# Optimization experiments

Measured on AMD Instinct MI355X. Metric: run time of the kernel, lower is better.

## Reference

```python
import jax, jax.numpy as jnp
import numpy as np

B, N, M, T, D, NH = 64, 1024, 32, 8, 512, 8
OUT = 1000
NSO, NSA = N // 4, N // 8
DH = D // NH


def _conv(x, w, b):
    y = jax.lax.conv_general_dilated(x, w, (1, 1), 'SAME', dimension_numbers=('NCHW', 'OIHW', 'NCHW'))
    return y + b[None, :, None, None]


def _bn(x, g, b):
    # BatchNorm2d in train mode: per-batch statistics over (B, H, W)
    m = x.mean(axis=(0, 2, 3), keepdims=True)
    v = x.var(axis=(0, 2, 3), keepdims=True)
    return (x - m) * jax.lax.rsqrt(v + 1e-5) * g[None, :, None, None] + b[None, :, None, None]


def _mp2(x):
    b_, c, h, w = x.shape
    return x.reshape(b_, c, h // 2, 2, w // 2, 2).max(axis=(3, 5))


def _ln(x, g, b):
    m = x.mean(-1, keepdims=True)
    v = x.var(-1, keepdims=True)
    return (x - m) * jax.lax.rsqrt(v + 1e-5) * g + b


def _glu(x):
    a, b = jnp.split(x, 2, axis=-1)
    return a * jax.nn.sigmoid(b)


def setup_inputs():
    ks = iter(jax.random.split(jax.random.key(0), 64))

    def nrm(shape, fan_in):
        return jax.random.normal(next(ks), shape, jnp.float32) / np.float32(np.sqrt(fan_in))

    inp = {}
    inp['x'] = jax.random.normal(next(ks), (B, 3, 64, 64), jnp.float32)
    inp['c1w'] = nrm((16, 3, 3, 3), 27); inp['c1b'] = jnp.zeros((16,))
    inp['bn1g'] = jnp.ones((16,)); inp['bn1b'] = jnp.zeros((16,))
    inp['c2w'] = nrm((32, 16, 3, 3), 144); inp['c2b'] = jnp.zeros((32,))
    inp['bn2g'] = jnp.ones((32,)); inp['bn2b'] = jnp.zeros((32,))
    inp['c3w'] = nrm((64, 32, 3, 3), 288); inp['c3b'] = jnp.zeros((64,))
    inp['bn3g'] = jnp.ones((64,)); inp['bn3b'] = jnp.zeros((64,))
    inp['c4w'] = nrm((64, 64, 3, 3), 576); inp['c4b'] = jnp.zeros((64,))
    inp['bn4g'] = jnp.ones((64,)); inp['bn4b'] = jnp.zeros((64,))
    inp['fc1w'] = nrm((256, 256), 256); inp['fc1b'] = jnp.zeros((256,))
    inp['fc2w'] = nrm((128, D), 128); inp['fc2b'] = jnp.zeros((D,))
    inp['kvw'] = nrm((D, D), D); inp['kvb'] = jnp.zeros((D,))
    inp['kvlg'] = jnp.ones((D,)); inp['kvlb'] = jnp.zeros((D,))
    inp['synw'] = nrm((D + N, 2 * N), D + N); inp['synb'] = jnp.zeros((2 * N,))
    inp['synlg'] = jnp.ones((N,)); inp['synlb'] = jnp.zeros((N,))
    inp['nlm_w1'] = nrm((N, M, 256), M); inp['nlm_b1'] = jnp.zeros((N, 256))
    inp['nlm_w2'] = nrm((N, 128), 128); inp['nlm_b2'] = jnp.zeros((N,))
    inp['start_act'] = nrm((N,), N)
    inp['start_trace'] = nrm((N, M), N + M)
    inp['dec_a'] = jax.random.uniform(next(ks), (NSA,), jnp.float32, 0.0, 3.0)
    inp['dec_o'] = jax.random.uniform(next(ks), (NSO,), jnp.float32, 0.0, 3.0)
    inp['qw'] = nrm((NSA, D), NSA); inp['qb'] = jnp.zeros((D,))
    inp['attn_inw'] = nrm((D, 3 * D), D); inp['attn_inb'] = jnp.zeros((3 * D,))
    inp['attn_ow'] = nrm((D, D), D); inp['attn_ob'] = jnp.zeros((D,))
    inp['op_w1'] = nrm((NSO, 256), NSO); inp['op_b1'] = jnp.zeros((256,))
    inp['op_l1g'] = jnp.ones((256,)); inp['op_l1b'] = jnp.zeros((256,))
    inp['op_w2'] = nrm((256, 64), 256); inp['op_b2'] = jnp.zeros((64,))
    inp['op_l2g'] = jnp.ones((64,)); inp['op_l2b'] = jnp.zeros((64,))
    inp['op_w3'] = nrm((64, OUT), 64); inp['op_b3'] = jnp.zeros((OUT,))
    inp['aL'] = jax.random.randint(next(ks), (NSA,), 0, N)
    inp['aR'] = jax.random.randint(next(ks), (NSA,), 0, N)
    inp['oL'] = jax.random.randint(next(ks), (NSO,), 0, N)
    inp['oR'] = jax.random.randint(next(ks), (NSO,), 0, N)
    inp['task_idx'] = 0
    return inp


def _forward(x, c1w, c1b, bn1g, bn1b, c2w, c2b, bn2g, bn2b, c3w, c3b, bn3g, bn3b, c4w, c4b, bn4g, bn4b, fc1w, fc1b, fc2w, fc2b, kvw, kvb, kvlg, kvlb, synw, synb, synlg, synlb, nlm_w1, nlm_b1, nlm_w2, nlm_b2, start_act, start_trace, dec_a, dec_o, qw, qb, attn_inw, attn_inb, attn_ow, attn_ob, op_w1, op_b1, op_l1g, op_l1b, op_w2, op_b2, op_l2g, op_l2b, op_w3, op_b3, aL, aR, oL, oR):
    # --- AdaptiveCNNEncoder (3-channel branch) ---
    h = jax.nn.relu(_bn(_conv(x, c1w, c1b), bn1g, bn1b))
    h = jax.nn.relu(_bn(_conv(h, c2w, c2b), bn2g, bn2b))
    h = _mp2(h)
    h = jax.nn.relu(_bn(_conv(h, c3w, c3b), bn3g, bn3b))
    h = _mp2(h)
    h = jax.nn.relu(_bn(_conv(h, c4w, c4b), bn4g, bn4b))
    b_, c, hh, ww = h.shape
    # AdaptiveAvgPool2d((2,2)): mean over equal blocks (16x16 -> 2x2)
    h = h.reshape(b_, c, 2, hh // 2, 2, ww // 2).mean(axis=(3, 5)).reshape(b_, c * 4)
    enc = _glu(h @ fc1w + fc1b) @ fc2w + fc2b            # (B, D)
    kv = _ln(enc @ kvw + kvb, kvlg, kvlb)                # single kv token

    Wq, Wk, Wv = jnp.split(attn_inw, 3, axis=1)
    bq, bk, bv = jnp.split(attn_inb, 3)
    kh = (kv @ Wk + bk).reshape(B, NH, DH)
    vh = (kv @ Wv + bv).reshape(B, NH, DH)

    r_a = jnp.exp(-jnp.clip(dec_a, 0.0, 15.0))           # (NSA,)
    r_o = jnp.exp(-jnp.clip(dec_o, 0.0, 15.0))           # (NSO,)

    act0 = jnp.broadcast_to(start_act, (B, N))
    trace0 = jnp.broadcast_to(start_trace, (B, N, M))
    ao0 = act0[:, oL] * act0[:, oR]                      # initial out-sync accumulators
    bo0 = jnp.ones_like(ao0)
    inv_log_out = np.float32(1.0 / np.log(OUT))
    inv_sqrt_dh = np.float32(1.0 / np.sqrt(DH))

    def tick(carry, t):
        act, trace, aa, ba, ao, bo = carry
        pp = act[:, aL] * act[:, aR]
        first = (t == 0)
        aa = jnp.where(first, pp, r_a * aa + pp)
        ba = jnp.where(first, jnp.ones_like(ba), r_a * ba + 1.0)
        sync_a = aa * jax.lax.rsqrt(ba + 1e-8)
        qv = sync_a @ qw + qb
        qh = (qv @ Wq + bq).reshape(B, NH, DH)
        logits = jnp.einsum('bhd,bhd->bh', qh, kh) * inv_sqrt_dh
        w = jax.nn.softmax(logits[..., None], axis=-1)[..., 0]  # single key -> ones
        attn_out = (w[..., None] * vh).reshape(B, D) @ attn_ow + attn_ob
        pre = jnp.concatenate([attn_out, act], axis=-1)
        state = _ln(_glu(pre @ synw + synb), synlg, synlb)
        trace = jnp.concatenate([trace[:, :, 1:], state[:, :, None]], axis=-1)
        # per-neuron private MLPs, batched: (B,N,M)x(N,M,256) -> GLU -> (N,128) -> scalar
        hid = _glu(jnp.einsum('bnm,nmh->bnh', trace, nlm_w1) + nlm_b1)
        act = jnp.einsum('bnh,nh->bn', hid, nlm_w2) + nlm_b2
        po = act[:, oL] * act[:, oR]
        ao = r_o * ao + po
        bo = r_o * bo + 1.0
        sync_o = ao * jax.lax.rsqrt(bo + 1e-8)
        h1 = jax.nn.relu(_ln(sync_o @ op_w1 + op_b1, op_l1g, op_l1b))
        h2 = jax.nn.relu(_ln(h1 @ op_w2 + op_b2, op_l2g, op_l2b))
        pred = h2 @ op_w3 + op_b3
        p = jax.nn.softmax(pred, axis=-1)
        ent = -jnp.sum(p * jnp.log(p + 1e-10), axis=-1)
        ne = ent * inv_log_out
        cert = jnp.stack([ne, 1.0 - ne], axis=-1)
        return (act, trace, aa, ba, ao, bo), (pred, cert)

    carry0 = (act0, trace0, jnp.zeros((B, NSA), jnp.float32), jnp.zeros((B, NSA), jnp.float32), ao0, bo0)
    _, (preds, certs) = jax.lax.scan(tick, carry0, jnp.arange(T))
    return jnp.transpose(preds, (1, 2, 0)), jnp.transpose(certs, (1, 2, 0))


def reference(x, c1w, c1b, bn1g, bn1b, c2w, c2b, bn2g, bn2b, c3w, c3b, bn3g, bn3b, c4w, c4b, bn4g, bn4b, fc1w, fc1b, fc2w, fc2b, kvw, kvb, kvlg, kvlb, synw, synb, synlg, synlb, nlm_w1, nlm_b1, nlm_w2, nlm_b2, start_act, start_trace, dec_a, dec_o, qw, qb, attn_inw, attn_inb, attn_ow, attn_ob, op_w1, op_b1, op_l1g, op_l1b, op_w2, op_b2, op_l2g, op_l2b, op_w3, op_b3, aL, aR, oL, oR, task_idx):
    del task_idx  # single task; all task-indexed params are for task 0
    return _forward(x, c1w, c1b, bn1g, bn1b, c2w, c2b, bn2g, bn2b, c3w, c3b, bn3g, bn3b, c4w, c4b, bn4g, bn4b, fc1w, fc1b, fc2w, fc2b, kvw, kvb, kvlg, kvlb, synw, synb, synlg, synlb, nlm_w1, nlm_b1, nlm_w2, nlm_b2, start_act, start_trace, dec_a, dec_o, qw, qb, attn_inw, attn_inb, attn_ow, attn_ob, op_w1, op_b1, op_l1g, op_l1b, op_w2, op_b2, op_l2g, op_l2b, op_w3, op_b3, aL, aR, oL, oR)
```

## Files before the change

kernel.cpp:

```cpp
#include <hip/hip_runtime.h>
#include <math.h>

constexpr int B_ = 64, N_ = 1024, M_ = 32, T_ = 8;
constexpr int OUT_ = 1000, NSO_ = 256;

#define DEVFN __device__ __forceinline__

typedef __attribute__((ext_vector_type(8))) short bf16x8;
typedef __attribute__((ext_vector_type(4))) float f32x4;

DEVFN float blockReduceSum(float v, float* buf) {
  int t = threadIdx.x;
  buf[t] = v; __syncthreads();
  for (int off = blockDim.x >> 1; off > 0; off >>= 1) {
    if (t < off) buf[t] += buf[t + off];
    __syncthreads();
  }
  float r = buf[0];
  __syncthreads();
  return r;
}

DEVFN float sigmoidf_(float x) { return 1.f / (1.f + __expf(-x)); }

DEVFN unsigned short f2bf(float f) {
  unsigned u = __float_as_uint(f);
  unsigned r = (u + 0x7FFFu + ((u >> 16) & 1u)) >> 16;
  return (unsigned short)r;
}
DEVFN float bf2f(unsigned short h) { return __uint_as_float((unsigned)h << 16); }

template<int NW>
DEVFN float bsum(float v, float* red) {
  #pragma unroll
  for (int o = 32; o > 0; o >>= 1) v += __shfl_xor(v, o);
  int w = threadIdx.x >> 6, ln = threadIdx.x & 63;
  if (ln == 0) red[w] = v;
  __syncthreads();
  if (w == 0) {
    float x = (ln < NW) ? red[ln] : 0.f;
    #pragma unroll
    for (int o = 8; o > 0; o >>= 1) x += __shfl_xor(x, o);
    if (ln == 0) red[0] = x;
  }
  __syncthreads();
  float r = red[0];
  __syncthreads();
  return r;
}

template<int NW>
DEVFN float bmax(float v, float* red) {
  #pragma unroll
  for (int o = 32; o > 0; o >>= 1) v = fmaxf(v, __shfl_xor(v, o));
  int w = threadIdx.x >> 6, ln = threadIdx.x & 63;
  if (ln == 0) red[w] = v;
  __syncthreads();
  if (w == 0) {
    float x = (ln < NW) ? red[ln] : -INFINITY;
    #pragma unroll
    for (int o = 8; o > 0; o >>= 1) x = fmaxf(x, __shfl_xor(x, o));
    if (ln == 0) red[0] = x;
  }
  __syncthreads();
  float r = red[0];
  __syncthreads();
  return r;
}

__global__ __launch_bounds__(256)
void k_w1t(const float* __restrict__ w1, unsigned short* __restrict__ w1t) {
  int n = blockIdx.x;
  __shared__ float tile[32][260];
  const float* src = w1 + (size_t)n * 8192;
  for (int i = threadIdx.x; i < 8192; i += 256)
    tile[i >> 8][i & 255] = src[i];
  __syncthreads();
  int c = threadIdx.x;
  unsigned short* dst = w1t + ((size_t)n * 256 + c) * 32;
  #pragma unroll
  for (int q = 0; q < 8; ++q) {
    ushort4 o;
    o.x = f2bf(tile[q * 4 + 0][c]); o.y = f2bf(tile[q * 4 + 1][c]);
    o.z = f2bf(tile[q * 4 + 2][c]); o.w = f2bf(tile[q * 4 + 3][c]);
    *reinterpret_cast<ushort4*>(dst + q * 4) = o;
  }
}

__global__ __launch_bounds__(256)
void k_synwt(const float* __restrict__ synw2, unsigned short* __restrict__ Bt) {
  int j0 = blockIdx.x * 64, k0 = blockIdx.y * 64;
  __shared__ float tile[64][65];
  for (int i = threadIdx.x; i < 4096; i += 256) {
    int kk = i >> 6, jj = i & 63;
    tile[kk][jj] = synw2[(size_t)(k0 + kk) * 2048 + j0 + jj];
  }
  __syncthreads();
  int jj = threadIdx.x >> 2, kq = (threadIdx.x & 3) * 16;
  unsigned short* dst = Bt + (size_t)(j0 + jj) * 1024 + k0 + kq;
  #pragma unroll
  for (int q = 0; q < 4; ++q) {
    ushort4 o;
    o.x = f2bf(tile[kq + q * 4 + 0][jj]); o.y = f2bf(tile[kq + q * 4 + 1][jj]);
    o.z = f2bf(tile[kq + q * 4 + 2][jj]); o.w = f2bf(tile[kq + q * 4 + 3][jj]);
    *reinterpret_cast<ushort4*>(dst + q * 4) = o;
  }
}

template<int CIN, int COUT, int HW, int TY, int XV, int CICH, int MODE, int KSPLIT, int COSPLIT>
__global__ __launch_bounds__(256)
void k_conv_tiled(const float* __restrict__ in, const float* __restrict__ wgl,
                  const float2* __restrict__ ssin, float* __restrict__ outp) {
  constexpr int XQ = HW / XV;
  constexpr int NCG = 4;
  constexpr int CPT = COUT / (NCG * COSPLIT);
  constexpr int PADW = HW + 8;
  constexpr int NROW = TY + 2;
  constexpr int CINB = CIN / KSPLIT;
  constexpr int NCH = CINB / CICH;
  static_assert(XQ * TY == 64, "spatial threads per co-group must be 64");
  __shared__ __align__(16) float ins[CICH][NROW][PADW];

  const int b   = blockIdx.x;
  const int y0  = blockIdx.y * TY;
  const int cs  = (COSPLIT > 1) ? (int)(blockIdx.z % COSPLIT) : 0;
  const int ks  = (KSPLIT > 1) ? (int)(blockIdx.z / COSPLIT) : 0;
  const int co0 = cs * (COUT / COSPLIT);
  const int tid = threadIdx.x;
  const int sp  = tid & 63;
  const int cg  = __builtin_amdgcn_readfirstlane(tid >> 6);
  const int xq  = sp % XQ;
  const int yr  = sp / XQ;
  const int x0  = xq * XV;

  float acc[CPT][XV];
  #pragma unroll
  for (int j = 0; j < CPT; ++j)
    #pragma unroll
    for (int k = 0; k < XV; ++k) acc[j][k] = 0.f;

  for (int ch = 0; ch < NCH; ++ch) {
    const int ci0 = ks * CINB + ch * CICH;
    __syncthreads();
    constexpr int NEL = CICH * NROW * PADW;
    for (int i = tid; i < NEL; i += 256) {
      int col = i % PADW;
      int row = (i / PADW) % NROW;
      int ci  = i / (PADW * NROW);
      int gx = col - 4;
      int gy = y0 + row - 1;
      float v = 0.f;
      if (gx >= 0 && gx < HW && gy >= 0 && gy < HW) {
        if (MODE == 0) {
          v = in[((size_t)(b * CIN + ci0 + ci) * HW + gy) * HW + gx];
        } else if (MODE == 1) {
          float2 s = ssin[ci0 + ci];
          v = fmaxf(fmaf(in[((size_t)(b * CIN + ci0 + ci) * HW + gy) * HW + gx], s.x, s.y), 0.f);
        } else {
          float2 s = ssin[ci0 + ci];
          const float* p = in + ((size_t)(b * CIN + ci0 + ci) * (2 * HW) + 2 * gy) * (2 * HW) + 2 * gx;
          float v0 = fmaf(p[0],          s.x, s.y);
          float v1 = fmaf(p[1],          s.x, s.y);
          float v2 = fmaf(p[2 * HW],     s.x, s.y);
          float v3 = fmaf(p[2 * HW + 1], s.x, s.y);
          v = fmaxf(fmaxf(fmaxf(v0, v1), fmaxf(v2, v3)), 0.f);
        }
      }
      ins[ci][row][col] = v;
    }
    __syncthreads();

    for (int ci = 0; ci < CICH; ++ci) {
      const float* wci = wgl + ((size_t)(co0 + cg * CPT) * CIN + (ci0 + ci)) * 9;
      #pragma unroll
      for (int dy = 0; dy < 3; ++dy) {
        const float* r = &ins[ci][yr + dy][x0 + 4];
        float win[XV + 2];
        win[0] = r[-1];
        if constexpr (XV == 4) {
          float4 m = *reinterpret_cast<const float4*>(r);
          win[1] = m.x; win[2] = m.y; win[3] = m.z; win[4] = m.w;
        } else if constexpr (XV == 2) {
          float2 m = *reinterpret_cast<const float2*>(r);
          win[1] = m.x; win[2] = m.y;
        } else {
          win[1] = r[0];
        }
        win[XV + 1] = r[XV];
        #pragma unroll
        for (int j = 0; j < CPT; ++j) {
          const float* wj = wci + (size_t)j * CIN * 9 + dy * 3;
          float w0 = wj[0], w1 = wj[1], w2 = wj[2];
          #pragma unroll
          for (int k = 0; k < XV; ++k)
            acc[j][k] = fmaf(win[k], w0, fmaf(win[k + 1], w1, fmaf(win[k + 2], w2, acc[j][k])));
        }
      }
    }
  }

  const size_t pofs = (size_t)ks * B_ * COUT * HW * HW;
  #pragma unroll
  for (int j = 0; j < CPT; ++j) {
    float* op = outp + pofs + (((size_t)b * COUT + co0 + cg * CPT + j) * HW + y0 + yr) * HW + x0;
    if constexpr (XV == 4)
      *reinterpret_cast<float4*>(op) = make_float4(acc[j][0], acc[j][1], acc[j][2], acc[j][3]);
    else if constexpr (XV == 2)
      *reinterpret_cast<float2*>(op) = make_float2(acc[j][0], acc[j][1]);
    else
      *op = acc[j][0];
  }
}

template<int C, int HW2, int NS>
__global__ __launch_bounds__(256)
void k_bn_stats(const float* __restrict__ x, float* __restrict__ part) {
  int c = blockIdx.x, s = blockIdx.y, ns = gridDim.y;
  const int Npc = B_ * HW2;
  constexpr size_t PSTR = (size_t)B_ * C * HW2;
  float s1 = 0.f, s2 = 0.f;
  for (int ii = s * 256 + threadIdx.x; ii < Npc; ii += ns * 256) {
    int b = ii / HW2, pos = ii % HW2;
    size_t base = ((size_t)b * C + c) * HW2 + pos;
    float v = x[base];
    #pragma unroll
    for (int q = 1; q < NS; ++q) v += x[base + q * PSTR];
    s1 += v; s2 += v * v;
  }
  __shared__ float r1[256], r2[256];
  r1[threadIdx.x] = s1; r2[threadIdx.x] = s2; __syncthreads();
  for (int off = 128; off > 0; off >>= 1) {
    if (threadIdx.x < off) { r1[threadIdx.x] += r1[threadIdx.x + off]; r2[threadIdx.x] += r2[threadIdx.x + off]; }
    __syncthreads();
  }
  if (threadIdx.x == 0) {
    part[(c * ns + s) * 2 + 0] = r1[0];
    part[(c * ns + s) * 2 + 1] = r2[0];
  }
}

__global__ void k_bn_finalize(const float* __restrict__ part, int C, int ns, float inv_n,
                              const float* __restrict__ g, const float* __restrict__ bb,
                              float2* __restrict__ ss) {
  int c = threadIdx.x;
  if (c >= C) return;
  float s1 = 0.f, s2 = 0.f;
  for (int s = 0; s < ns; ++s) { s1 += part[(c * ns + s) * 2]; s2 += part[(c * ns + s) * 2 + 1]; }
  float m = s1 * inv_n;
  float var = s2 * inv_n - m * m;
  float rstd = rsqrtf(var + 1e-5f);
  float sc = g[c] * rstd;
  ss[c] = make_float2(sc, bb[c] - m * sc);
}

__global__ __launch_bounds__(256)
void k_avgpool_bn(const float* __restrict__ x, const float2* __restrict__ ss,
                  float* __restrict__ outp) {
  constexpr size_t PSTR = (size_t)B_ * 64 * 256;
  int idx = blockIdx.x * 256 + threadIdx.x;
  if (idx >= B_ * 256) return;
  int b = idx >> 8;
  int r = idx & 255;
  int c = r >> 2, i = (r >> 1) & 1, j = r & 1;
  float2 s = ss[c];
  const float* p = x + ((size_t)(b * 64 + c) * 16 + i * 8) * 16 + j * 8;
  float sum = 0.f;
  #pragma unroll
  for (int yy = 0; yy < 8; ++yy)
    #pragma unroll
    for (int xx = 0; xx < 8; ++xx) {
      size_t o = yy * 16 + xx;
      float v = p[o] + p[o + PSTR] + p[o + 2 * PSTR] + p[o + 3 * PSTR];
      sum += fmaxf(fmaf(v, s.x, s.y), 0.f);
    }
  outp[idx] = sum * (1.f / 64.f);
}

template<int K, int NOUT>
__global__ __launch_bounds__(256)
void k_gemm_part(const float* __restrict__ A, const float* __restrict__ W, int ldw,
                 float* __restrict__ part) {
  int jt = blockIdx.x, ks = blockIdx.y;
  int k0 = ks * 64;
  __shared__ float As[64][65];
  for (int i = threadIdx.x; i < 4096; i += 256) {
    int r = i >> 6, c = i & 63;
    As[r][c] = A[(size_t)r * K + k0 + c];
  }
  __syncthreads();
  int jsub = threadIdx.x & 31;
  int bg = threadIdx.x >> 5;
  int j = jt * 32 + jsub;
  float acc[8] = {0.f, 0.f, 0.f, 0.f, 0.f, 0.f, 0.f, 0.f};
  const float* wp = W + (size_t)k0 * ldw + j;
  #pragma unroll 8
  for (int kk = 0; kk < 64; ++kk) {
    float w = wp[(size_t)kk * ldw];
    #pragma unroll
    for (int r = 0; r < 8; ++r) acc[r] = fmaf(As[bg * 8 + r][kk], w, acc[r]);
  }
  float* pp = part + (size_t)ks * 64 * NOUT + j;
  #pragma unroll
  for (int r = 0; r < 8; ++r) pp[(size_t)(bg * 8 + r) * NOUT] = acc[r];
}

__global__ __launch_bounds__(256)
void k_syn_mfma(const unsigned short* __restrict__ Abf, const unsigned short* __restrict__ Bt,
                float* __restrict__ part) {
  const int jt = blockIdx.x, ks = blockIdx.y;
  const int w = threadIdx.x >> 6, lane = threadIdx.x & 63;
  const int col = lane & 15, kg = lane >> 4;
  const int jcol = jt * 64 + w * 16 + col;
  const int k0 = ks * 256;
  f32x4 acc[4];
  #pragma unroll
  for (int mt = 0; mt < 4; ++mt) acc[mt] = (f32x4){0.f, 0.f, 0.f, 0.f};

  #pragma unroll
  for (int kb = 0; kb < 8; ++kb) {
    const int kk = k0 + kb * 32 + kg * 8;
    bf16x8 bfr = *reinterpret_cast<const bf16x8*>(Bt + (size_t)jcol * 1024 + kk);
    #pragma unroll
    for (int mt = 0; mt < 4; ++mt) {
      bf16x8 a = *reinterpret_cast<const bf16x8*>(Abf + (size_t)(mt * 16 + col) * 1024 + kk);
      acc[mt] = __builtin_amdgcn_mfma_f32_16x16x32_bf16(a, bfr, acc[mt], 0, 0, 0);
    }
  }
  #pragma unroll
  for (int mt = 0; mt < 4; ++mt) {
    int b0 = mt * 16 + kg * 4;
    #pragma unroll
    for (int r = 0; r < 4; ++r)
      part[((size_t)ks * 64 + b0 + r) * 2048 + jcol] = acc[mt][r];
  }
}

template<int NOUT, int NO_FIN, int KS, bool GLU_, bool LN_>
__global__ __launch_bounds__(256)
void k_fc_reduce(const float* __restrict__ part, const float* __restrict__ bias, int bstride,
                 const float* __restrict__ lng, const float* __restrict__ lnb,
                 float* __restrict__ outp) {
  constexpr int R = (NO_FIN + 255) / 256;
  int b = blockIdx.x, t = threadIdx.x;
  const float* bp = bias + (size_t)b * bstride;
  float v[R];
  #pragma unroll
  for (int r = 0; r < R; ++r) {
    int j = t + r * 256;
    if (j < NO_FIN) {
      float za = bp[j];
      float zb = GLU_ ? bp[j + NO_FIN] : 0.f;
      #pragma unroll
      for (int ks = 0; ks < KS; ++ks) {
        const float* pr = part + ((size_t)ks * 64 + b) * NOUT;
        za += pr[j];
        if (GLU_) zb += pr[j + NO_FIN];
      }
      v[r] = GLU_ ? za * sigmoidf_(zb) : za;
    } else v[r] = 0.f;
  }
  if (LN_) {
    __shared__ float red[256];
    float s1 = 0.f, s2 = 0.f;
    #pragma unroll
    for (int r = 0; r < R; ++r) { s1 += v[r]; s2 += v[r] * v[r]; }
    s1 = blockReduceSum(s1, red);
    s2 = blockReduceSum(s2, red);
    float mu = s1 / (float)NO_FIN;
    float rstd = rsqrtf(s2 / (float)NO_FIN - mu * mu + 1e-5f);
    #pragma unroll
    for (int r = 0; r < R; ++r) {
      int j = t + r * 256;
      if (j < NO_FIN) outp[(size_t)b * NO_FIN + j] = fmaf((v[r] - mu) * rstd, lng[j], lnb[j]);
    }
  } else {
    #pragma unroll
    for (int r = 0; r < R; ++r) {
      int j = t + r * 256;
      if (j < NO_FIN) outp[(size_t)b * NO_FIN + j] = v[r];
    }
  }
}

__global__ __launch_bounds__(1024)
void k_syn_reduce(const float* __restrict__ part, const float* __restrict__ syncst,
                  const float* __restrict__ g, const float* __restrict__ bb,
                  unsigned short* __restrict__ trace, int slot) {
  int b = blockIdx.x, t = threadIdx.x;
  __shared__ float red[16];
  float za = syncst[b * 2048 + t];
  float zb = syncst[b * 2048 + 1024 + t];
  #pragma unroll
  for (int ks = 0; ks < 4; ++ks) {
    const float* pr = part + ((size_t)ks * 64 + b) * 2048;
    za += pr[t];
    zb += pr[t + 1024];
  }
  float v = za * sigmoidf_(zb);
  float s1 = bsum<16>(v, red);
  float s2 = bsum<16>(v * v, red);
  float mu = s1 * (1.f / 1024.f);
  float rstd = rsqrtf(s2 * (1.f / 1024.f) - mu * mu + 1e-5f);
  trace[((size_t)t * 64 + b) * 32 + slot] = f2bf(fmaf((v - mu) * rstd, g[t], bb[t]));
}

__global__ __launch_bounds__(256)
void k_init(const float* __restrict__ sa, const float* __restrict__ st,
            const int* __restrict__ oL, const int* __restrict__ oR,
            float* __restrict__ act, unsigned short* __restrict__ act_bf,
            unsigned short* __restrict__ trace,
            float* __restrict__ ao, float* __restrict__ bo) {
  int idx = blockIdx.x * 256 + threadIdx.x;
  if (idx < B_ * N_ * M_) {
    int n = idx >> 11, m = idx & 31;
    trace[idx] = f2bf(st[n * 32 + m]);
  }
  if (idx < B_ * N_) {
    float v = sa[idx % N_];
    act[idx] = v;
    act_bf[idx] = f2bf(v);
  }
  if (idx < B_ * NSO_) {
    int i = idx % NSO_;
    ao[idx] = sa[oL[i]] * sa[oR[i]];
    bo[idx] = 1.f;
  }
}

__global__ __launch_bounds__(128)
void k_nlm_mfma(const unsigned short* __restrict__ trace, const unsigned short* __restrict__ w1t,
                const float* __restrict__ b1, const float* __restrict__ w2,
                const float* __restrict__ b2, float* __restrict__ act,
                unsigned short* __restrict__ act_bf, int tick) {
  const int w = threadIdx.x >> 6, lane = threadIdx.x & 63;
  const int n = blockIdx.x * 2 + w;
  const int col = lane & 15, kg = lane >> 4;
  __shared__ __align__(16) unsigned short ldsA[2][64][40];
  {
    const uint4* src = reinterpret_cast<const uint4*>(trace + ((size_t)n * 64 + lane) * 32);
    uint4 r0 = src[0], r1 = src[1], r2 = src[2], r3 = src[3];
    uint4* d = reinterpret_cast<uint4*>(&ldsA[w][lane][0]);
    d[0] = r0; d[1] = r1; d[2] = r2; d[3] = r3;
  }
  bf16x8 bf[16];
  float b1v[16], w2v[8];
  #pragma unroll
  for (int nt = 0; nt < 16; ++nt) {
    bf[nt] = *reinterpret_cast<const bf16x8*>(w1t + (((size_t)n * 256 + nt * 16 + col) * 32 + kg * 8));
    b1v[nt] = b1[n * 256 + nt * 16 + col];
  }
  #pragma unroll
  for (int nt = 0; nt < 8; ++nt) w2v[nt] = w2[n * 128 + nt * 16 + col];
  const float b2n = b2[n];
  const int kbase = kg * 8 + ((tick + 1) & 31);
  __syncthreads();
  #pragma unroll
  for (int mt = 0; mt < 4; ++mt) {
    const int brow = mt * 16 + col;
    bf16x8 af;
    #pragma unroll
    for (int j = 0; j < 8; ++j)
      af[j] = (short)ldsA[w][brow][(kbase + j) & 31];
    f32x4 acc[16];
    #pragma unroll
    for (int nt = 0; nt < 16; ++nt)
      acc[nt] = __builtin_amdgcn_mfma_f32_16x16x32_bf16(af, bf[nt], (f32x4){0.f, 0.f, 0.f, 0.f}, 0, 0, 0);
    float v0 = 0.f, v1 = 0.f, v2 = 0.f, v3 = 0.f;
    #pragma unroll
    for (int nt = 0; nt < 8; ++nt) {
      f32x4 za = acc[nt], zb = acc[nt + 8];
// ... 18 lines not shown
      act_bf[(size_t)(b0 + 0) * 1024 + n] = f2bf(r0);
      act_bf[(size_t)(b0 + 1) * 1024 + n] = f2bf(r1);
      act_bf[(size_t)(b0 + 2) * 1024 + n] = f2bf(r2);
      act_bf[(size_t)(b0 + 3) * 1024 + n] = f2bf(r3);
    }
  }
}

__global__ __launch_bounds__(1024)
void k_outpath(const float* __restrict__ act, float* __restrict__ ao, float* __restrict__ bo,
               const float* __restrict__ dec_o, const int* __restrict__ oL, const int* __restrict__ oR,
               const float* __restrict__ opw1, const float* __restrict__ opb1,
               const float* __restrict__ l1g, const float* __restrict__ l1b,
               const float* __restrict__ opw2, const float* __restrict__ opb2,
               const float* __restrict__ l2g, const float* __restrict__ l2b,
               const float* __restrict__ opw3, const float* __restrict__ opb3,
               float* __restrict__ outp, int tick) {
  int b = blockIdx.x, t = threadIdx.x;
  __shared__ float red[16];
  __shared__ float syo[256], h1s[256], h2s[64];
  __shared__ float zp1[4][256];
  __shared__ float zp2[16][64];
  const float* actb = act + (size_t)b * 1024;
  if (t < 256) {
    float po = actb[oL[t]] * actb[oR[t]];
    float r = __expf(-fminf(fmaxf(dec_o[t], 0.f), 15.f));
    int ai = b * 256 + t;
    float av = fmaf(r, ao[ai], po);
    float bv = fmaf(r, bo[ai], 1.f);
    ao[ai] = av; bo[ai] = bv;
    syo[t] = av * rsqrtf(bv + 1e-8f);
  }
  __syncthreads();
  {
    int j = t & 255, ks = t >> 8;
    float z = 0.f;
    const float* wcol = opw1 + j;
    #pragma unroll 8
    for (int k = ks * 64; k < ks * 64 + 64; ++k) z = fmaf(syo[k], wcol[k * 256], z);
    zp1[ks][j] = z;
  }
  __syncthreads();
  float h1v = 0.f;
  if (t < 256) h1v = zp1[0][t] + zp1[1][t] + zp1[2][t] + zp1[3][t] + opb1[t];
  float s1 = bsum<16>(t < 256 ? h1v : 0.f, red);
  float s2 = bsum<16>(t < 256 ? h1v * h1v : 0.f, red);
  if (t < 256) {
    float mu = s1 * (1.f / 256.f);
    float rstd = rsqrtf(s2 * (1.f / 256.f) - mu * mu + 1e-5f);
    h1s[t] = fmaxf(fmaf((h1v - mu) * rstd, l1g[t], l1b[t]), 0.f);
  }
  __syncthreads();
  {
    int j = t & 63, ks = t >> 6;
    float z = 0.f;
    const float* wcol = opw2 + j;
    #pragma unroll
    for (int k = ks * 16; k < ks * 16 + 16; ++k) z = fmaf(h1s[k], wcol[k * 64], z);
    zp2[ks][j] = z;
  }
  __syncthreads();
  if (t < 64) {
    float z2 = opb2[t];
    #pragma unroll
    for (int ks = 0; ks < 16; ++ks) z2 += zp2[ks][t];
    float a1 = z2, a2 = z2 * z2;
    #pragma unroll
    for (int o = 32; o > 0; o >>= 1) { a1 += __shfl_xor(a1, o); a2 += __shfl_xor(a2, o); }
    float mu2 = a1 * (1.f / 64.f);
    float rs2 = rsqrtf(a2 * (1.f / 64.f) - mu2 * mu2 + 1e-5f);
    h2s[t] = fmaxf(fmaf((z2 - mu2) * rs2, l2g[t], l2b[t]), 0.f);
  }
  __syncthreads();
  float z3 = 0.f;
  if (t < OUT_) {
    z3 = opb3[t];
    const float* wcol = opw3 + t;
    #pragma unroll 8
    for (int k = 0; k < 64; ++k) z3 = fmaf(h2s[k], wcol[k * OUT_], z3);
    outp[(size_t)b * (OUT_ * T_) + (size_t)t * T_ + tick] = z3;
  }
  float mx = bmax<16>(t < OUT_ ? z3 : -INFINITY, red);
  float e = (t < OUT_) ? __expf(z3 - mx) : 0.f;
  float S = bsum<16>(e, red);
  float inv = 1.f / S;
  float ep = 0.f;
  if (t < OUT_) {
    float p = e * inv;
    ep = p * __logf(p + 1e-10f);
  }
  float ent = -bsum<16>(ep, red);
  if (t == 0) {
    float ne = ent * (1.f / logf(1000.f));
    outp[(size_t)B_ * OUT_ * T_ + (size_t)b * 2 * T_ + tick]      = ne;
    outp[(size_t)B_ * OUT_ * T_ + (size_t)b * 2 * T_ + T_ + tick] = 1.f - ne;
  }
}

extern "C" void kernel_launch(void* const* d_in, const int* in_sizes, int n_in,
                              void* d_out, int out_size, void* d_ws, size_t ws_size,
                              hipStream_t stream) {
  (void)in_sizes; (void)n_in; (void)out_size; (void)ws_size;
  const float* x      = (const float*)d_in[0];
  const float* c1w    = (const float*)d_in[1];
  const float* bn1g   = (const float*)d_in[3];
  const float* bn1b   = (const float*)d_in[4];
  const float* c2w    = (const float*)d_in[5];
  const float* bn2g   = (const float*)d_in[7];
  const float* bn2b   = (const float*)d_in[8];
  const float* c3w    = (const float*)d_in[9];
  const float* bn3g   = (const float*)d_in[11];
  const float* bn3b   = (const float*)d_in[12];
  const float* c4w    = (const float*)d_in[13];
  const float* bn4g   = (const float*)d_in[15];
  const float* bn4b   = (const float*)d_in[16];
  const float* fc1w   = (const float*)d_in[17];
  const float* fc1b   = (const float*)d_in[18];
  const float* fc2w   = (const float*)d_in[19];
  const float* fc2b   = (const float*)d_in[20];
  const float* kvw    = (const float*)d_in[21];
  const float* kvb    = (const float*)d_in[22];
  const float* kvlg   = (const float*)d_in[23];
  const float* kvlb   = (const float*)d_in[24];
  const float* synw   = (const float*)d_in[25];
  const float* synb   = (const float*)d_in[26];
  const float* synlg  = (const float*)d_in[27];
  const float* synlb  = (const float*)d_in[28];
  const float* nlmw1  = (const float*)d_in[29];
  const float* nlmb1  = (const float*)d_in[30];
  const float* nlmw2  = (const float*)d_in[31];
  const float* nlmb2  = (const float*)d_in[32];
  const float* sact   = (const float*)d_in[33];
  const float* strc   = (const float*)d_in[34];
  const float* dec_o  = (const float*)d_in[36];
  const float* attn_inw = (const float*)d_in[39];
  const float* attn_inb = (const float*)d_in[40];
  const float* attn_ow  = (const float*)d_in[41];
  const float* attn_ob  = (const float*)d_in[42];
  const float* opw1   = (const float*)d_in[43];
  const float* opb1   = (const float*)d_in[44];
  const float* opl1g  = (const float*)d_in[45];
  const float* opl1b  = (const float*)d_in[46];
  const float* opw2   = (const float*)d_in[47];
  const float* opb2   = (const float*)d_in[48];
  const float* opl2g  = (const float*)d_in[49];
  const float* opl2b  = (const float*)d_in[50];
  const float* opw3   = (const float*)d_in[51];
  const float* opb3   = (const float*)d_in[52];
  const int*   oL     = (const int*)d_in[55];
  const int*   oR     = (const int*)d_in[56];
  float* outp = (float*)d_out;
  float* ws   = (float*)d_ws;

  float* c2raw = ws;
  float* c4part= ws;
  float* c1raw = ws + 8388608;
  float* c3raw = ws + 8388608;
  float* part  = ws + 4194304;
  unsigned short* trace_bf = (unsigned short*)(ws + 6291456);
  float* act   = ws + 8388608;
  float* syncst= ws + 8454144;
  float* pooled= ws + 8585216;
  float* ench  = ws + 8601600;
  float* enc   = ws + 8609792;
  float* kvbuf = ws + 8642560;
  float* vhbuf = ws + 8675328;
  float* aout  = ws + 8708096;
  float* ao    = ws + 8740864;
  float* bo    = ws + 8757248;
  unsigned short* w1t_bf   = (unsigned short*)(ws + 8777728);
  unsigned short* synw2t_bf= (unsigned short*)(ws + 12972032);
  float* bnpart= ws + 14020608;
  float2* bnss = (float2*)(ws + 14024704);
  unsigned short* act_bf = (unsigned short*)(ws + 14028800);

  k_conv_tiled<3,16,64,4,4,3,0,1,1><<<dim3(64,16),256,0,stream>>>(x, c1w, nullptr, c1raw);
  k_bn_stats<16,4096,1><<<dim3(16,32),256,0,stream>>>(c1raw, bnpart);
  k_bn_finalize<<<1,64,0,stream>>>(bnpart, 16, 32, 1.f/(float)(B_*4096), bn1g, bn1b, bnss);

  k_conv_tiled<16,32,64,2,2,16,1,1,1><<<dim3(64,32),256,0,stream>>>(c1raw, c2w, bnss, c2raw);
  k_bn_stats<32,4096,1><<<dim3(32,32),256,0,stream>>>(c2raw, bnpart);
  k_bn_finalize<<<1,64,0,stream>>>(bnpart, 32, 32, 1.f/(float)(B_*4096), bn2g, bn2b, bnss);

  k_conv_tiled<32,64,32,4,2,16,2,1,2><<<dim3(64,8,2),256,0,stream>>>(c2raw, c3w, bnss, c3raw);
  k_bn_stats<64,1024,1><<<dim3(64,16),256,0,stream>>>(c3raw, bnpart);
  k_bn_finalize<<<1,64,0,stream>>>(bnpart, 64, 16, 1.f/(float)(B_*1024), bn3g, bn3b, bnss);

  k_conv_tiled<64,64,16,4,1,16,2,4,1><<<dim3(64,4,4),256,0,stream>>>(c3raw, c4w, bnss, c4part);

  k_w1t<<<1024,256,0,stream>>>(nlmw1, w1t_bf);
  k_synwt<<<dim3(32,16),256,0,stream>>>(synw + (size_t)512 * 2048, synw2t_bf);

  k_bn_stats<64,256,4><<<dim3(64,8),256,0,stream>>>(c4part, bnpart);
  k_bn_finalize<<<1,64,0,stream>>>(bnpart, 64, 8, 1.f/(float)(B_*256), bn4g, bn4b, bnss);
  k_avgpool_bn<<<64,256,0,stream>>>(c4part, bnss, pooled);

  k_gemm_part<256,256><<<dim3(8,4),256,0,stream>>>(pooled, fc1w, 256, part);
  k_fc_reduce<256,128,4,true,false><<<64,256,0,stream>>>(part, fc1b, 0, nullptr, nullptr, ench);
  k_gemm_part<128,512><<<dim3(16,2),256,0,stream>>>(ench, fc2w, 512, part);
  k_fc_reduce<512,512,2,false,false><<<64,256,0,stream>>>(part, fc2b, 0, nullptr, nullptr, enc);
  k_gemm_part<512,512><<<dim3(16,8),256,0,stream>>>(enc, kvw, 512, part);
  k_fc_reduce<512,512,8,false,true><<<64,256,0,stream>>>(part, kvb, 0, kvlg, kvlb, kvbuf);
  k_gemm_part<512,512><<<dim3(16,8),256,0,stream>>>(kvbuf, attn_inw + 1024, 1536, part);
  k_fc_reduce<512,512,8,false,false><<<64,256,0,stream>>>(part, attn_inb + 1024, 0, nullptr, nullptr, vhbuf);
  k_gemm_part<512,512><<<dim3(16,8),256,0,stream>>>(vhbuf, attn_ow, 512, part);
  k_fc_reduce<512,512,8,false,false><<<64,256,0,stream>>>(part, attn_ob, 0, nullptr, nullptr, aout);
  k_gemm_part<512,2048><<<dim3(64,8),256,0,stream>>>(aout, synw, 2048, part);
  k_fc_reduce<2048,2048,8,false,false><<<64,256,0,stream>>>(part, synb, 0, nullptr, nullptr, syncst);

  k_init<<<8192,256,0,stream>>>(sact, strc, oL, oR, act, act_bf, trace_bf, ao, bo);

  for (int t = 0; t < T_; ++t) {
    k_syn_mfma<<<dim3(32,4),256,0,stream>>>(act_bf, synw2t_bf, part);
    k_syn_reduce<<<64,1024,0,stream>>>(part, syncst, synlg, synlb, trace_bf, t);
    k_nlm_mfma<<<512,128,0,stream>>>(trace_bf, w1t_bf, nlmb1, nlmw2, nlmb2, act, act_bf, t);
    k_outpath<<<64,1024,0,stream>>>(act, ao, bo, dec_o, oL, oR,
                                    opw1, opb1, opl1g, opl1b,
                                    opw2, opb2, opl2g, opl2b,
                                    opw3, opb3, outp, t);
  }
}
```

Baseline: 595.2 us.

## Move conv2-4 to bf16 MFMA implicit GEMM with bf16 activations

```diff
diff --git a/kernel.cpp b/kernel.cpp
--- a/kernel.cpp
+++ b/kernel.cpp
@@ -68,6 +68,38 @@
   return r;
 }
 
+DEVFN void bn_ssl(float2* ssl, const float* bnpart, const float* g, const float* bb,
+                  int C, int ns, float inv_n) {
+  for (int c = threadIdx.x; c < C; c += blockDim.x) {
+    float s1 = 0.f, s2 = 0.f;
+    for (int s = 0; s < ns; ++s) { s1 += bnpart[(c * ns + s) * 2]; s2 += bnpart[(c * ns + s) * 2 + 1]; }
+    float m = s1 * inv_n;
+    float var = s2 * inv_n - m * m;
+    float rstd = rsqrtf(var + 1e-5f);
+    float sc = g[c] * rstd;
+    ssl[c] = make_float2(sc, bb[c] - m * sc);
+  }
+}
+
+__global__ __launch_bounds__(256)
+void k_wprep(const float* __restrict__ c2w, const float* __restrict__ c3w,
+             const float* __restrict__ c4w, unsigned short* __restrict__ wt2,
+             unsigned short* __restrict__ wt3, unsigned short* __restrict__ wt4) {
+  int i = blockIdx.x * 256 + threadIdx.x;
+  if (i < 5120) {
+    int tap = i / 512, co = (i / 16) % 32, ci = i & 15;
+    wt2[i] = (tap < 9) ? f2bf(c2w[(co * 16 + ci) * 9 + tap]) : 0;
+  } else if (i < 5120 + 18432) {
+    int j = i - 5120;
+    int tap = j / 2048, co = (j / 32) % 64, ci = j & 31;
+    wt3[j] = f2bf(c3w[(co * 32 + ci) * 9 + tap]);
+  } else if (i < 5120 + 18432 + 36864) {
+    int j = i - 5120 - 18432;
+    int tap = j / 4096, co = (j / 64) % 64, ci = j & 63;
+    wt4[j] = f2bf(c4w[(co * 64 + ci) * 9 + tap]);
+  }
+}
+
 __global__ __launch_bounds__(256)
 void k_w1t(const float* __restrict__ w1, unsigned short* __restrict__ w1t) {
   int n = blockIdx.x;
@@ -107,125 +139,221 @@
   }
 }
 
-template<int CIN, int COUT, int HW, int TY, int XV, int CICH, int MODE, int KSPLIT, int COSPLIT>
-__global__ __launch_bounds__(256)
-void k_conv_tiled(const float* __restrict__ in, const float* __restrict__ wgl,
-                  const float2* __restrict__ ssin, float* __restrict__ outp) {
-  constexpr int XQ = HW / XV;
-  constexpr int NCG = 4;
-  constexpr int CPT = COUT / (NCG * COSPLIT);
-  constexpr int PADW = HW + 8;
-  constexpr int NROW = TY + 2;
-  constexpr int CINB = CIN / KSPLIT;
-  constexpr int NCH = CINB / CICH;
-  static_assert(XQ * TY == 64, "spatial threads per co-group must be 64");
-  __shared__ __align__(16) float ins[CICH][NROW][PADW];
-
-  const int b   = blockIdx.x;
-  const int y0  = blockIdx.y * TY;
-  const int cs  = (COSPLIT > 1) ? (int)(blockIdx.z % COSPLIT) : 0;
-  const int ks  = (KSPLIT > 1) ? (int)(blockIdx.z / COSPLIT) : 0;
-  const int co0 = cs * (COUT / COSPLIT);
+__global__ __launch_bounds__(256)
+void k_conv1(const float* __restrict__ in, const float* __restrict__ wgl,
+             unsigned short* __restrict__ outp) {
+  constexpr int HW = 64, TY = 4, XV = 4, XQ = 16, CPT = 4;
+  __shared__ __align__(16) float ins[3][TY + 2][HW + 8];
+  const int b = blockIdx.x, y0 = blockIdx.y * TY, tid = threadIdx.x;
+  const int sp = tid & 63;
+  const int cg = __builtin_amdgcn_readfirstlane(tid >> 6);
+  const int xq = sp % XQ, yr = sp / XQ, x0 = xq * XV;
+  float acc[CPT][XV];
+  #pragma unroll
+  for (int j = 0; j < CPT; ++j)
+    #pragma unroll
+    for (int k = 0; k < XV; ++k) acc[j][k] = 0.f;
+  constexpr int NEL = 3 * (TY + 2) * (HW + 8);
+  for (int i = tid; i < NEL; i += 256) {
+    int col = i % (HW + 8), row = (i / (HW + 8)) % (TY + 2), ci = i / ((HW + 8) * (TY + 2));
+    int gx = col - 4, gy = y0 + row - 1;
+    float v = 0.f;
+    if (gx >= 0 && gx < HW && gy >= 0 && gy < HW)
+      v = in[((size_t)(b * 3 + ci) * HW + gy) * HW + gx];
+    ins[ci][row][col] = v;
+  }
+  __syncthreads();
+  for (int ci = 0; ci < 3; ++ci) {
+    const float* wci = wgl + ((size_t)(cg * CPT) * 3 + ci) * 9;
+    #pragma unroll
+    for (int dy = 0; dy < 3; ++dy) {
+      const float* r = &ins[ci][yr + dy][x0 + 4];
+      float win[6];
+      win[0] = r[-1];
+      float4 m = *reinterpret_cast<const float4*>(r);
+      win[1] = m.x; win[2] = m.y; win[3] = m.z; win[4] = m.w;
+      win[5] = r[4];
+      #pragma unroll
+      for (int j = 0; j < CPT; ++j) {
+        const float* wj = wci + (size_t)j * 27 + dy * 3;
+        float w0 = wj[0], w1 = wj[1], w2 = wj[2];
+        #pragma unroll
+        for (int k = 0; k < XV; ++k)
+          acc[j][k] = fmaf(win[k], w0, fmaf(win[k + 1], w1, fmaf(win[k + 2], w2, acc[j][k])));
+      }
+    }
+  }
+  #pragma unroll
+  for (int j = 0; j < CPT; ++j) {
+    unsigned short* op = outp + (((size_t)b * 16 + cg * CPT + j) * HW + y0 + yr) * HW + x0;
+    ushort4 o;
+    o.x = f2bf(acc[j][0]); o.y = f2bf(acc[j][1]); o.z = f2bf(acc[j][2]); o.w = f2bf(acc[j][3]);
+    *reinterpret_cast<ushort4*>(op) = o;
+  }
+}
+
+__global__ __launch_bounds__(256)
+void k_conv2_mfma(const unsigned short* __restrict__ in, const unsigned short* __restrict__ wt2,
+                  const float* __restrict__ bnpart, const float* __restrict__ bng,
+                  const float* __restrict__ bnb, unsigned short* __restrict__ outp) {
+  const int b = blockIdx.x, y = blockIdx.y;
   const int tid = threadIdx.x;
-  const int sp  = tid & 63;
-  const int cg  = __builtin_amdgcn_readfirstlane(tid >> 6);
-  const int xq  = sp % XQ;
-  const int yr  = sp / XQ;
-  const int x0  = xq * XV;
-
-  float acc[CPT][XV];
-  #pragma unroll
-  for (int j = 0; j < CPT; ++j)
-    #pragma unroll
-    for (int k = 0; k < XV; ++k) acc[j][k] = 0.f;
-
-  for (int ch = 0; ch < NCH; ++ch) {
-    const int ci0 = ks * CINB + ch * CICH;
-    __syncthreads();
-    constexpr int NEL = CICH * NROW * PADW;
-    for (int i = tid; i < NEL; i += 256) {
-      int col = i % PADW;
-      int row = (i / PADW) % NROW;
-      int ci  = i / (PADW * NROW);
-      int gx = col - 4;
-      int gy = y0 + row - 1;
-      float v = 0.f;
-      if (gx >= 0 && gx < HW && gy >= 0 && gy < HW) {
-        if (MODE == 0) {
-          v = in[((size_t)(b * CIN + ci0 + ci) * HW + gy) * HW + gx];
-        } else if (MODE == 1) {
-          float2 s = ssin[ci0 + ci];
-          v = fmaxf(fmaf(in[((size_t)(b * CIN + ci0 + ci) * HW + gy) * HW + gx], s.x, s.y), 0.f);
-        } else {
-          float2 s = ssin[ci0 + ci];
-          const float* p = in + ((size_t)(b * CIN + ci0 + ci) * (2 * HW) + 2 * gy) * (2 * HW) + 2 * gx;
-          float v0 = fmaf(p[0],          s.x, s.y);
-          float v1 = fmaf(p[1],          s.x, s.y);
-          float v2 = fmaf(p[2 * HW],     s.x, s.y);
-          float v3 = fmaf(p[2 * HW + 1], s.x, s.y);
-          v = fmaxf(fmaxf(fmaxf(v0, v1), fmaxf(v2, v3)), 0.f);
-        }
+  const int w = tid >> 6, lane = tid & 63;
+  const int col = lane & 15, kg = lane >> 4;
+  const int p0 = w * 16;
+  __shared__ unsigned short lds[3][68][16];
+  __shared__ float2 ssl[16];
+  bn_ssl(ssl, bnpart, bng, bnb, 16, 32, 1.f / (float)(B_ * 4096));
+  __syncthreads();
+  for (int i = tid; i < 3 * 66 * 16; i += 256) {
+    int px = i % 66, row = (i / 66) % 3, ci = i / 198;
+    int gy = y + row - 1, gx = px - 1;
+    float v = 0.f;
+    if (gy >= 0 && gy < 64 && gx >= 0 && gx < 64) {
+      float2 s = ssl[ci];
+      v = fmaxf(fmaf(bf2f(in[((size_t)(b * 16 + ci) * 64 + gy) * 64 + gx]), s.x, s.y), 0.f);
+    }
+    lds[row][px][ci] = f2bf(v);
+  }
+  __syncthreads();
+  f32x4 acc0 = {0.f, 0.f, 0.f, 0.f}, acc1 = {0.f, 0.f, 0.f, 0.f};
+  const int tsel = kg >> 1, ci0 = (kg & 1) * 8;
+  #pragma unroll
+  for (int p = 0; p < 5; ++p) {
+    int tap = 2 * p + tsel;
+    int dy = (tap < 9) ? tap / 3 : 0;
+    int dx = (tap < 9) ? tap % 3 : 0;
+    bf16x8 af = *reinterpret_cast<const bf16x8*>(&lds[dy][p0 + col + dx][ci0]);
+    bf16x8 b0 = *reinterpret_cast<const bf16x8*>(wt2 + ((size_t)tap * 32 + col) * 16 + ci0);
+    bf16x8 b1 = *reinterpret_cast<const bf16x8*>(wt2 + ((size_t)tap * 32 + 16 + col) * 16 + ci0);
+    acc0 = __builtin_amdgcn_mfma_f32_16x16x32_bf16(af, b0, acc0, 0, 0, 0);
+    acc1 = __builtin_amdgcn_mfma_f32_16x16x32_bf16(af, b1, acc1, 0, 0, 0);
+  }
+  int px = p0 + kg * 4;
+  ushort4 o0, o1;
+  o0.x = f2bf(acc0[0]); o0.y = f2bf(acc0[1]); o0.z = f2bf(acc0[2]); o0.w = f2bf(acc0[3]);
+  o1.x = f2bf(acc1[0]); o1.y = f2bf(acc1[1]); o1.z = f2bf(acc1[2]); o1.w = f2bf(acc1[3]);
+  *reinterpret_cast<ushort4*>(outp + ((size_t)(b * 32 + col) * 64 + y) * 64 + px) = o0;
+  *reinterpret_cast<ushort4*>(outp + ((size_t)(b * 32 + 16 + col) * 64 + y) * 64 + px) = o1;
+}
+
+__global__ __launch_bounds__(256)
+void k_conv3_mfma(const unsigned short* __restrict__ in, const unsigned short* __restrict__ wt3,
+                  const float* __restrict__ bnpart, const float* __restrict__ bng,
+                  const float* __restrict__ bnb, unsigned short* __restrict__ outp) {
+  const int b = blockIdx.x, y0 = blockIdx.y * 2;
+  const int tid = threadIdx.x;
+  const int w = tid >> 6, lane = tid & 63;
+  const int col = lane & 15, kg = lane >> 4;
+  const int yloc = w >> 1, p0 = (w & 1) * 16;
+  __shared__ unsigned short lds[4][34][40];
+  __shared__ float2 ssl[32];
+  bn_ssl(ssl, bnpart, bng, bnb, 32, 32, 1.f / (float)(B_ * 4096));
+  __syncthreads();
+  for (int i = tid; i < 4 * 34 * 32; i += 256) {
+    int px = i % 34, row = (i / 34) % 4, ci = i / 136;
+    int gy = y0 + row - 1, gx = px - 1;
+    float v = 0.f;
+    if (gy >= 0 && gy < 32 && gx >= 0 && gx < 32) {
+      float2 s = ssl[ci];
+      size_t base = ((size_t)(b * 32 + ci) * 64 + 2 * gy) * 64 + 2 * gx;
+      float r0 = fmaf(bf2f(in[base]),      s.x, s.y);
+      float r1 = fmaf(bf2f(in[base + 1]),  s.x, s.y);
+      float r2 = fmaf(bf2f(in[base + 64]), s.x, s.y);
+      float r3 = fmaf(bf2f(in[base + 65]), s.x, s.y);
+      v = fmaxf(fmaxf(fmaxf(r0, r1), fmaxf(r2, r3)), 0.f);
+    }
+    lds[row][px][ci] = f2bf(v);
+  }
+  __syncthreads();
+  f32x4 acc[4];
+  #pragma unroll
+  for (int c = 0; c < 4; ++c) acc[c] = (f32x4){0.f, 0.f, 0.f, 0.f};
+  #pragma unroll
+  for (int tap = 0; tap < 9; ++tap) {
+    int dy = tap / 3, dx = tap % 3;
+    bf16x8 af = *reinterpret_cast<const bf16x8*>(&lds[yloc + dy][p0 + col + dx][kg * 8]);
+    #pragma unroll
+    for (int c = 0; c < 4; ++c) {
+      bf16x8 bfr = *reinterpret_cast<const bf16x8*>(wt3 + ((size_t)tap * 64 + c * 16 + col) * 32 + kg * 8);
+      acc[c] = __builtin_amdgcn_mfma_f32_16x16x32_bf16(af, bfr, acc[c], 0, 0, 0);
+    }
+  }
+  int yy = y0 + yloc, px = p0 + kg * 4;
+  #pragma unroll
+  for (int c = 0; c < 4; ++c) {
+    ushort4 o;
+    o.x = f2bf(acc[c][0]); o.y = f2bf(acc[c][1]); o.z = f2bf(acc[c][2]); o.w = f2bf(acc[c][3]);
+    *reinterpret_cast<ushort4*>(outp + ((size_t)(b * 64 + c * 16 + col) * 32 + yy) * 32 + px) = o;
+  }
+}
+
+__global__ __launch_bounds__(128)
+void k_conv4_mfma(const unsigned short* __restrict__ in, const unsigned short* __restrict__ wt4,
+                  const float* __restrict__ bnpart, const float* __restrict__ bng,
+                  const float* __restrict__ bnb, unsigned short* __restrict__ outp) {
+  const int b = blockIdx.x, y0 = blockIdx.y * 2;
+  const int tid = threadIdx.x;
+  const int w = tid >> 6, lane = tid & 63;
+  const int col = lane & 15, kg = lane >> 4;
+  __shared__ unsigned short lds[4][18][72];
+  __shared__ float2 ssl[64];
+  bn_ssl(ssl, bnpart, bng, bnb, 64, 16, 1.f / (float)(B_ * 1024));
+  __syncthreads();
+  for (int i = tid; i < 4 * 18 * 64; i += 128) {
+    int px = i % 18, row = (i / 18) % 4, ci = i / 72;
+    int gy = y0 + row - 1, gx = px - 1;
+    float v = 0.f;
+    if (gy >= 0 && gy < 16 && gx >= 0 && gx < 16) {
+      float2 s = ssl[ci];
+      size_t base = ((size_t)(b * 64 + ci) * 32 + 2 * gy) * 32 + 2 * gx;
+      float r0 = fmaf(bf2f(in[base]),      s.x, s.y);
+      float r1 = fmaf(bf2f(in[base + 1]),  s.x, s.y);
+      float r2 = fmaf(bf2f(in[base + 32]), s.x, s.y);
+      float r3 = fmaf(bf2f(in[base + 33]), s.x, s.y);
+      v = fmaxf(fmaxf(fmaxf(r0, r1), fmaxf(r2, r3)), 0.f);
+    }
+    lds[row][px][ci] = f2bf(v);
+  }
+  __syncthreads();
+  f32x4 acc[4];
+  #pragma unroll
+  for (int c = 0; c < 4; ++c) acc[c] = (f32x4){0.f, 0.f, 0.f, 0.f};
+  #pragma unroll
+  for (int tap = 0; tap < 9; ++tap) {
+    int dy = tap / 3, dx = tap % 3;
+    #pragma unroll
+    for (int kc = 0; kc < 2; ++kc) {
+      bf16x8 af = *reinterpret_cast<const bf16x8*>(&lds[w + dy][col + dx][kc * 32 + kg * 8]);
+      #pragma unroll
+      for (int c = 0; c < 4; ++c) {
+        bf16x8 bfr = *reinterpret_cast<const bf16x8*>(wt4 + ((size_t)tap * 64 + c * 16 + col) * 64 + kc * 32 + kg * 8);
+        acc[c] = __builtin_amdgcn_mfma_f32_16x16x32_bf16(af, bfr, acc[c], 0, 0, 0);
       }
-      ins[ci][row][col] = v;
-    }
-    __syncthreads();
-
-    for (int ci = 0; ci < CICH; ++ci) {
-      const float* wci = wgl + ((size_t)(co0 + cg * CPT) * CIN + (ci0 + ci)) * 9;
-      #pragma unroll
-      for (int dy = 0; dy < 3; ++dy) {
-        const float* r = &ins[ci][yr + dy][x0 + 4];
-        float win[XV + 2];
-        win[0] = r[-1];
-        if constexpr (XV == 4) {
-          float4 m = *reinterpret_cast<const float4*>(r);
-          win[1] = m.x; win[2] = m.y; win[3] = m.z; win[4] = m.w;
-        } else if constexpr (XV == 2) {
-          float2 m = *reinterpret_cast<const float2*>(r);
-          win[1] = m.x; win[2] = m.y;
-        } else {
-          win[1] = r[0];
-        }
-        win[XV + 1] = r[XV];
-        #pragma unroll
-        for (int j = 0; j < CPT; ++j) {
-          const float* wj = wci + (size_t)j * CIN * 9 + dy * 3;
-          float w0 = wj[0], w1 = wj[1], w2 = wj[2];
-          #pragma unroll
-          for (int k = 0; k < XV; ++k)
-            acc[j][k] = fmaf(win[k], w0, fmaf(win[k + 1], w1, fmaf(win[k + 2], w2, acc[j][k])));
-        }
-      }
-    }
-  }
-
-  const size_t pofs = (size_t)ks * B_ * COUT * HW * HW;
-  #pragma unroll
-  for (int j = 0; j < CPT; ++j) {
-    float* op = outp + pofs + (((size_t)b * COUT + co0 + cg * CPT + j) * HW + y0 + yr) * HW + x0;
-    if constexpr (XV == 4)
-      *reinterpret_cast<float4*>(op) = make_float4(acc[j][0], acc[j][1], acc[j][2], acc[j][3]);
-    else if constexpr (XV == 2)
-      *reinterpret_cast<float2*>(op) = make_float2(acc[j][0], acc[j][1]);
-    else
-      *op = acc[j][0];
-  }
-}
-
-template<int C, int HW2, int NS>
-__global__ __launch_bounds__(256)
-void k_bn_stats(const float* __restrict__ x, float* __restrict__ part) {
+    }
+  }
+  int yy = y0 + w, px = kg * 4;
+  #pragma unroll
+  for (int c = 0; c < 4; ++c) {
+    ushort4 o;
+    o.x = f2bf(acc[c][0]); o.y = f2bf(acc[c][1]); o.z = f2bf(acc[c][2]); o.w = f2bf(acc[c][3]);
+    *reinterpret_cast<ushort4*>(outp + ((size_t)(b * 64 + c * 16 + col) * 16 + yy) * 16 + px) = o;
+  }
+}
+
+template<int C, int HW2>
+__global__ __launch_bounds__(256)
+void k_bn_stats_bf(const unsigned short* __restrict__ x, float* __restrict__ part) {
   int c = blockIdx.x, s = blockIdx.y, ns = gridDim.y;
-  const int Npc = B_ * HW2;
-  constexpr size_t PSTR = (size_t)B_ * C * HW2;
+  const int Np2 = B_ * HW2 / 2;
   float s1 = 0.f, s2 = 0.f;
-  for (int ii = s * 256 + threadIdx.x; ii < Npc; ii += ns * 256) {
-    int b = ii / HW2, pos = ii % HW2;
-    size_t base = ((size_t)b * C + c) * HW2 + pos;
-    float v = x[base];
-    #pragma unroll
-    for (int q = 1; q < NS; ++q) v += x[base + q * PSTR];
-    s1 += v; s2 += v * v;
+  for (int ii = s * 256 + threadIdx.x; ii < Np2; ii += ns * 256) {
+    int b = ii / (HW2 / 2), p2 = ii % (HW2 / 2);
+    const unsigned short* pp = x + ((size_t)b * C + c) * HW2 + p2 * 2;
+    unsigned u = *reinterpret_cast<const unsigned*>(pp);
+    float v0 = __uint_as_float(u << 16);
+    float v1 = __uint_as_float(u & 0xFFFF0000u);
+    s1 += v0 + v1; s2 += v0 * v0 + v1 * v1;
   }
   __shared__ float r1[256], r2[256];
   r1[threadIdx.x] = s1; r2[threadIdx.x] = s2; __syncthreads();
@@ -239,40 +367,25 @@
   }
 }
 
-__global__ void k_bn_finalize(const float* __restrict__ part, int C, int ns, float inv_n,
-                              const float* __restrict__ g, const float* __restrict__ bb,
-                              float2* __restrict__ ss) {
-  int c = threadIdx.x;
-  if (c >= C) return;
-  float s1 = 0.f, s2 = 0.f;
-  for (int s = 0; s < ns; ++s) { s1 += part[(c * ns + s) * 2]; s2 += part[(c * ns + s) * 2 + 1]; }
-  float m = s1 * inv_n;
-  float var = s2 * inv_n - m * m;
-  float rstd = rsqrtf(var + 1e-5f);
-  float sc = g[c] * rstd;
-  ss[c] = make_float2(sc, bb[c] - m * sc);
-}
-
-__global__ __launch_bounds__(256)
-void k_avgpool_bn(const float* __restrict__ x, const float2* __restrict__ ss,
-                  float* __restrict__ outp) {
-  constexpr size_t PSTR = (size_t)B_ * 64 * 256;
+__global__ __launch_bounds__(256)
+void k_avgpool_bn_bf(const unsigned short* __restrict__ x, const float* __restrict__ bnpart,
+                     const float* __restrict__ g, const float* __restrict__ bb,
+                     float* __restrict__ outp) {
+  __shared__ float2 ssl[64];
+  bn_ssl(ssl, bnpart, g, bb, 64, 8, 1.f / (float)(B_ * 256));
+  __syncthreads();
   int idx = blockIdx.x * 256 + threadIdx.x;
-  if (idx >= B_ * 256) return;
   int b = idx >> 8;
   int r = idx & 255;
   int c = r >> 2, i = (r >> 1) & 1, j = r & 1;
-  float2 s = ss[c];
-  const float* p = x + ((size_t)(b * 64 + c) * 16 + i * 8) * 16 + j * 8;
+  float2 s = ssl[c];
+  const unsigned short* p = x + ((size_t)(b * 64 + c) * 16 + i * 8) * 16 + j * 8;
   float sum = 0.f;
   #pragma unroll
   for (int yy = 0; yy < 8; ++yy)
     #pragma unroll
-    for (int xx = 0; xx < 8; ++xx) {
-      size_t o = yy * 16 + xx;
-      float v = p[o] + p[o + PSTR] + p[o + 2 * PSTR] + p[o + 3 * PSTR];
-      sum += fmaxf(fmaf(v, s.x, s.y), 0.f);
-    }
+    for (int xx = 0; xx < 8; ++xx)
+      sum += fmaxf(fmaf(bf2f(p[yy * 16 + xx]), s.x, s.y), 0.f);
   outp[idx] = sum * (1.f / 64.f);
 }
 
@@ -315,7 +428,6 @@
   f32x4 acc[4];
   #pragma unroll
   for (int mt = 0; mt < 4; ++mt) acc[mt] = (f32x4){0.f, 0.f, 0.f, 0.f};
-
   #pragma unroll
   for (int kb = 0; kb < 8; ++kb) {
     const int kk = k0 + kb * 32 + kg * 8;
@@ -640,10 +752,10 @@
   float* outp = (float*)d_out;
   float* ws   = (float*)d_ws;
 
-  float* c2raw = ws;
-  float* c4part= ws;
-  float* c1raw = ws + 8388608;
-  float* c3raw = ws + 8388608;
+  unsigned short* c1raw_bf = (unsigned short*)(ws + 8388608);
+  unsigned short* c2raw_bf = (unsigned short*)ws;
+  unsigned short* c3raw_bf = (unsigned short*)(ws + 8388608);
+  unsigned short* c4raw_bf = (unsigned short*)ws;
   float* part  = ws + 4194304;
   unsigned short* trace_bf = (unsigned short*)(ws + 6291456);
   float* act   = ws + 8388608;
@@ -658,30 +770,30 @@
   float* bo    = ws + 8757248;
   unsigned short* w1t_bf   = (unsigned short*)(ws + 8777728);
   unsigned short* synw2t_bf= (unsigned short*)(ws + 12972032);
-  float* bnpart= ws + 14020608;
-  float2* bnss = (float2*)(ws + 14024704);
-  unsigned short* act_bf = (unsigned short*)(ws + 14028800);
-
-  k_conv_tiled<3,16,64,4,4,3,0,1,1><<<dim3(64,16),256,0,stream>>>(x, c1w, nullptr, c1raw);
-  k_bn_stats<16,4096,1><<<dim3(16,32),256,0,stream>>>(c1raw, bnpart);
-  k_bn_finalize<<<1,64,0,stream>>>(bnpart, 16, 32, 1.f/(float)(B_*4096), bn1g, bn1b, bnss);
-
-  k_conv_tiled<16,32,64,2,2,16,1,1,1><<<dim3(64,32),256,0,stream>>>(c1raw, c2w, bnss, c2raw);
-  k_bn_stats<32,4096,1><<<dim3(32,32),256,0,stream>>>(c2raw, bnpart);
-  k_bn_finalize<<<1,64,0,stream>>>(bnpart, 32, 32, 1.f/(float)(B_*4096), bn2g, bn2b, bnss);
-
-  k_conv_tiled<32,64,32,4,2,16,2,1,2><<<dim3(64,8,2),256,0,stream>>>(c2raw, c3w, bnss, c3raw);
-  k_bn_stats<64,1024,1><<<dim3(64,16),256,0,stream>>>(c3raw, bnpart);
-  k_bn_finalize<<<1,64,0,stream>>>(bnpart, 64, 16, 1.f/(float)(B_*1024), bn3g, bn3b, bnss);
-
-  k_conv_tiled<64,64,16,4,1,16,2,4,1><<<dim3(64,4,4),256,0,stream>>>(c3raw, c4w, bnss, c4part);
+  unsigned short* wt2 = (unsigned short*)(ws + 14061568);
+  unsigned short* wt3 = (unsigned short*)(ws + 14064128);
+  unsigned short* wt4 = (unsigned short*)(ws + 14073344);
+  float* bnpart = ws + 14091776;
+  unsigned short* act_bf = (unsigned short*)(ws + 14095872);
+
+  k_wprep<<<236,256,0,stream>>>(c2w, c3w, c4w, wt2, wt3, wt4);
+
+  k_conv1<<<dim3(64,16),256,0,stream>>>(x, c1w, c1raw_bf);
+  k_bn_stats_bf<16,4096><<<dim3(16,32),256,0,stream>>>(c1raw_bf, bnpart);
+
+  k_conv2_mfma<<<dim3(64,64),256,0,stream>>>(c1raw_bf, wt2, bnpart, bn1g, bn1b, c2raw_bf);
+  k_bn_stats_bf<32,4096><<<dim3(32,32),256,0,stream>>>(c2raw_bf, bnpart);
+
+  k_conv3_mfma<<<dim3(64,16),256,0,stream>>>(c2raw_bf, wt3, bnpart, bn2g, bn2b, c3raw_bf);
+  k_bn_stats_bf<64,1024><<<dim3(64,16),256,0,stream>>>(c3raw_bf, bnpart);
+
+  k_conv4_mfma<<<dim3(64,8),128,0,stream>>>(c3raw_bf, wt4, bnpart, bn3g, bn3b, c4raw_bf);
 
   k_w1t<<<1024,256,0,stream>>>(nlmw1, w1t_bf);
   k_synwt<<<dim3(32,16),256,0,stream>>>(synw + (size_t)512 * 2048, synw2t_bf);
 
-  k_bn_stats<64,256,4><<<dim3(64,8),256,0,stream>>>(c4part, bnpart);
-  k_bn_finalize<<<1,64,0,stream>>>(bnpart, 64, 8, 1.f/(float)(B_*256), bn4g, bn4b, bnss);
-  k_avgpool_bn<<<64,256,0,stream>>>(c4part, bnss, pooled);
+  k_bn_stats_bf<64,256><<<dim3(64,8),256,0,stream>>>(c4raw_bf, bnpart);
+  k_avgpool_bn_bf<<<64,256,0,stream>>>(c4raw_bf, bnpart, bn4g, bn4b, pooled);
 
   k_gemm_part<256,256><<<dim3(8,4),256,0,stream>>>(pooled, fc1w, 256, part);
   k_fc_reduce<256,128,4,true,false><<<64,256,0,stream>>>(part, fc1b, 0, nullptr, nullptr, ench);
```

New measurement: 527.0 us. 1.13x faster.
